# Optimization experiments

Hardware: AMD Instinct MI355X
Metric: run time of the kernel (lower is better)

Reference implementation:

```python
import jax, jax.numpy as jnp
import numpy as np

N_NODES = 50000
N_EDGES = 600000
D_IN, F1, F2, F3, D_OUT = 128, 128, 64, 64, 32
N_GRAPHS = 512


def setup_inputs() -> dict:
    key = jax.random.key(0)
    ks = jax.random.split(key, 16)
    x = jax.random.normal(ks[0], (N_NODES, D_IN), dtype=jnp.float32)
    edge_index = jax.random.randint(ks[1], (2, N_EDGES), 0, N_NODES, dtype=jnp.int64)
    batch = jnp.sort(jax.random.randint(ks[2], (N_NODES,), 0, N_GRAPHS, dtype=jnp.int64))

    def lin(k, fan_in, fan_out):
        bound = 1.0 / np.sqrt(fan_in)
        return jax.random.uniform(k, (fan_out, fan_in), jnp.float32, -bound, bound)

    return {
        "x": x, "edge_index": edge_index, "batch": batch,
        "w1_rel": lin(ks[3], D_IN, F1), "b1": jnp.zeros((F1,), jnp.float32), "w1_root": lin(ks[4], D_IN, F1),
        "w2_rel": lin(ks[5], F1, F2), "b2": jnp.zeros((F2,), jnp.float32), "w2_root": lin(ks[6], F1, F2),
        "w3_rel": lin(ks[7], F2, F3), "b3": jnp.zeros((F3,), jnp.float32), "w3_root": lin(ks[8], F2, F3),
        "fc1_w": lin(ks[9], F3, F3), "fc1_b": jnp.zeros((F3,), jnp.float32),
        "fc2_w": lin(ks[10], F3, D_OUT), "fc2_b": jnp.zeros((D_OUT,), jnp.float32),
    }


def graph_conv(x, src, dst, w_rel, b_rel, w_root):
    # GraphConv: out_i = W_rel @ (sum_{j->i} x_j) + b + W_root @ x_i
    aggr = jax.ops.segment_sum(x[src], dst, num_segments=x.shape[0])  # [N, d]
    return aggr @ w_rel.T + b_rel + x @ w_root.T


def reference(x, edge_index, batch,
              w1_rel, b1, w1_root, w2_rel, b2, w2_root, w3_rel, b3, w3_root,
              fc1_w, fc1_b, fc2_w, fc2_b):
    src, dst = edge_index[0], edge_index[1]
    h = jax.nn.relu(graph_conv(x, src, dst, w1_rel, b1, w1_root))
    h = jax.nn.relu(graph_conv(h, src, dst, w2_rel, b2, w2_root))
    h = graph_conv(h, src, dst, w3_rel, b3, w3_root)
    # global_add_pool over graphs in the batch
    g = jax.ops.segment_sum(h, batch, num_segments=N_GRAPHS)  # [G, F3]
    t = jax.nn.relu(g @ fc1_w.T + fc1_b)
    scores = t @ fc2_w.T + fc2_b
    return jax.nn.log_softmax(scores, axis=-1)
```

## Files before the change

### kernel.cpp

```cpp
#include <hip/hip_runtime.h>

#define N_NODES  50000
#define N_EDGES  600000
#define N_GRAPHS 512

#define SCAN_N   (N_NODES + 1)
#define SCAN_BPB 1024
#define SCAN_NB  ((SCAN_N + SCAN_BPB - 1) / SCAN_BPB)

#define F2BF_BLOCKS 6250
#define ZR_BLOCKS   196
#define WC_BLOCKS   224
#define ZG_BLOCKS   128

typedef __attribute__((ext_vector_type(8))) short bf16x8;
typedef __attribute__((ext_vector_type(4))) float f32x4;

static __device__ __forceinline__ unsigned f2bf(float f) {
    unsigned u = __float_as_uint(f);
    return (u + 0x7FFFu + ((u >> 16) & 1u)) >> 16;
}
static __device__ __forceinline__ float bflo(unsigned v) { return __uint_as_float(v << 16); }
static __device__ __forceinline__ float bfhi(unsigned v) { return __uint_as_float(v & 0xFFFF0000u); }

static __device__ __forceinline__ void addv8(float* acc, uint4 v) {
    acc[0] += bflo(v.x); acc[1] += bfhi(v.x);
    acc[2] += bflo(v.y); acc[3] += bfhi(v.y);
    acc[4] += bflo(v.z); acc[5] += bfhi(v.z);
    acc[6] += bflo(v.w); acc[7] += bfhi(v.w);
}
static __device__ __forceinline__ uint4 packv8(const float* f) {
    uint4 o;
    o.x = f2bf(f[0]) | (f2bf(f[1]) << 16);
    o.y = f2bf(f[2]) | (f2bf(f[3]) << 16);
    o.z = f2bf(f[4]) | (f2bf(f[5]) << 16);
    o.w = f2bf(f[6]) | (f2bf(f[7]) << 16);
    return o;
}


__global__ void init_kernel(const float* __restrict__ x, uint2* __restrict__ xb,
                            int* __restrict__ rowptr,
                            const float* __restrict__ w1r, const float* __restrict__ w1o,
                            const float* __restrict__ w2r, const float* __restrict__ w2o,
                            const float* __restrict__ w3r, const float* __restrict__ w3o,
                            unsigned short* __restrict__ wdst, float* __restrict__ G) {
    int b = blockIdx.x, t = threadIdx.x;
    if (b < F2BF_BLOCKS) {
        int i = b * 256 + t;
        float4 v = ((const float4*)x)[i];
        uint2 o;
        o.x = f2bf(v.x) | (f2bf(v.y) << 16);
        o.y = f2bf(v.z) | (f2bf(v.w) << 16);
        xb[i] = o;
    } else if (b < F2BF_BLOCKS + ZR_BLOCKS) {
        int i = (b - F2BF_BLOCKS) * 256 + t;
        if (i < SCAN_N) rowptr[i] = 0;
    } else if (b < F2BF_BLOCKS + ZR_BLOCKS + WC_BLOCKS) {
        int i = (b - F2BF_BLOCKS - ZR_BLOCKS) * 256 + t;
        const float* src; int off;
        if      (i < 16384) { src = w1r; off = 0; }
        else if (i < 32768) { src = w1o; off = 16384; }
        else if (i < 40960) { src = w2r; off = 32768; }
        else if (i < 49152) { src = w2o; off = 40960; }
        else if (i < 53248) { src = w3r; off = 49152; }
        else if (i < 57344) { src = w3o; off = 53248; }
        else return;
        wdst[i] = (unsigned short)f2bf(src[i - off]);
    } else {
        int i = (b - F2BF_BLOCKS - ZR_BLOCKS - WC_BLOCKS) * 256 + t;
        G[i] = 0.f;
    }
}


__global__ void hist_kernel(const int* __restrict__ edge, int* __restrict__ rowptr) {
    int e = blockIdx.x * blockDim.x + threadIdx.x;
    if (e < N_EDGES) atomicAdd(&rowptr[edge[N_EDGES + e] + 1], 1);
}

__global__ void scan_reduce_kernel(const int* __restrict__ data, int* __restrict__ bsum) {
    __shared__ int red[256];
    int b = blockIdx.x, t = threadIdx.x;
    int base = b * SCAN_BPB + t * 4;
    int s = 0;
#pragma unroll
    for (int j = 0; j < 4; ++j) {
        int idx = base + j;
        if (idx < SCAN_N) s += data[idx];
    }
    red[t] = s;
    __syncthreads();
    for (int off = 128; off > 0; off >>= 1) {
        if (t < off) red[t] += red[t + off];
        __syncthreads();
    }
    if (t == 0) bsum[b] = red[0];
}

__global__ void scan_apply_kernel(int* __restrict__ data, const int* __restrict__ bsum,
                                  int* __restrict__ cursor) {
    __shared__ int th[256];
    __shared__ int boff;
    int b = blockIdx.x, t = threadIdx.x;
    if (t == 0) {
        int run = 0;
        for (int i = 0; i < b; ++i) run += bsum[i];
        boff = run;
    }
    int base = b * SCAN_BPB + t * 4;
    int v[4];
    int s = 0;
#pragma unroll
    for (int j = 0; j < 4; ++j) {
        int idx = base + j;
        v[j] = (idx < SCAN_N) ? data[idx] : 0;
        s += v[j];
    }
    th[t] = s;
    __syncthreads();
    for (int off = 1; off < 256; off <<= 1) {
        int x = (t >= off) ? th[t - off] : 0;
        __syncthreads();
        th[t] += x;
        __syncthreads();
    }
    int run = boff + th[t] - s;
#pragma unroll
    for (int j = 0; j < 4; ++j) {
        int idx = base + j;
        run += v[j];
        if (idx < SCAN_N) {
            data[idx] = run;
            if (idx < N_NODES) cursor[idx] = run;
        }
    }
}

__global__ void scatter_kernel(const int* __restrict__ edge, int* __restrict__ cursor,
                               int* __restrict__ csr) {
    int e = blockIdx.x * blockDim.x + threadIdx.x;
    if (e < N_EDGES) {
        int d = edge[N_EDGES + e];
        int p = atomicAdd(&cursor[d], 1);
        csr[p] = edge[e];
    }
}


template <int LPN>
__global__ void aggregate_root(const unsigned short* __restrict__ Xb,
                               const int* __restrict__ rowptr,
                               const int* __restrict__ csr,
                               const unsigned short* __restrict__ ROOT,
                               unsigned short* __restrict__ OUT) {
    constexpr int NPB = 256 / LPN;
    int grp = threadIdx.x / LPN, lane = threadIdx.x % LPN;
    int i = blockIdx.x * NPB + grp;
    if (i >= N_NODES) return;
    const uint4* __restrict__ X4 = (const uint4*)Xb;
    int s = rowptr[i], e = rowptr[i + 1];
    float a[8] = {0.f}, b[8] = {0.f};
    int p = s;
    for (; p + 4 <= e; p += 4) {
        uint4 v0 = X4[(size_t)csr[p + 0] * LPN + lane];
        uint4 v1 = X4[(size_t)csr[p + 1] * LPN + lane];
        uint4 v2 = X4[(size_t)csr[p + 2] * LPN + lane];
        uint4 v3 = X4[(size_t)csr[p + 3] * LPN + lane];
        addv8(a, v0); addv8(b, v1); addv8(a, v2); addv8(b, v3);
    }
    if (p + 2 <= e) {
        uint4 v0 = X4[(size_t)csr[p] * LPN + lane];
        uint4 v1 = X4[(size_t)csr[p + 1] * LPN + lane];
        addv8(a, v0); addv8(b, v1);
        p += 2;
    }
    if (p < e) {
        uint4 v = X4[(size_t)csr[p] * LPN + lane];
        addv8(a, v);
    }
    float f[8];
#pragma unroll
    for (int k = 0; k < 8; ++k) f[k] = a[k] + b[k];
    uint4 r = ((const uint4*)ROOT)[(size_t)i * LPN + lane];
    f[0] += bflo(r.x); f[1] += bfhi(r.x);
    f[2] += bflo(r.y); f[3] += bfhi(r.y);
    f[4] += bflo(r.z); f[5] += bfhi(r.z);
    f[6] += bflo(r.w); f[7] += bfhi(r.w);
    ((uint4*)OUT)[(size_t)i * LPN + lane] = packv8(f);
}

__launch_bounds__(256, 2)
__global__ void fused_l1(const unsigned short* __restrict__ XB,
                         const int* __restrict__ rowptr, const int* __restrict__ csr,
                         const unsigned short* __restrict__ W1,
                         const unsigned short* __restrict__ W2,
                         const float* __restrict__ bias,
                         unsigned short* __restrict__ OUT) {
    __shared__ unsigned short aggr[64 * 128];
    const int tid = threadIdx.x;
    const int i0 = blockIdx.x * 64;

    {
        const uint4* __restrict__ X4 = (const uint4*)XB;
        int grp = tid >> 4, lane = tid & 15;
        for (int j = 0; j < 4; ++j) {
            int row = grp * 4 + j;
            int i = i0 + row;
            if (i >= N_NODES) break;
            int s = rowptr[i], e = rowptr[i + 1];
            float a[8] = {0.f}, b[8] = {0.f};
            int p = s;
            for (; p + 4 <= e; p += 4) {
                uint4 v0 = X4[(size_t)csr[p + 0] * 16 + lane];
                uint4 v1 = X4[(size_t)csr[p + 1] * 16 + lane];
                uint4 v2 = X4[(size_t)csr[p + 2] * 16 + lane];
                uint4 v3 = X4[(size_t)csr[p + 3] * 16 + lane];
                addv8(a, v0); addv8(b, v1); addv8(a, v2); addv8(b, v3);
            }
            if (p + 2 <= e) {
                uint4 v0 = X4[(size_t)csr[p] * 16 + lane];
                uint4 v1 = X4[(size_t)csr[p + 1] * 16 + lane];
                addv8(a, v0); addv8(b, v1);
                p += 2;
            }
            if (p < e) { uint4 v = X4[(size_t)csr[p] * 16 + lane]; addv8(a, v); }
            float f[8];
#pragma unroll
            for (int k = 0; k < 8; ++k) f[k] = a[k] + b[k];
            *(uint4*)&aggr[(row * 16 + (lane ^ (row & 7))) * 8] = packv8(f);
        }
    }
    const int l = tid & 63, wv = tid >> 6;
    const int lm = l & 15, lk = l >> 4;
    const int colbase = wv * 32;
    bf16x8 wf[2][8];
#pragma unroll
    for (int t = 0; t < 2; ++t) {
        int wrow = colbase + t * 16 + lm;
#pragma unroll
        for (int ks = 0; ks < 4; ++ks)
            wf[t][ks] = *(const bf16x8*)(W1 + (size_t)wrow * 128 + ks * 32 + lk * 8);
#pragma unroll
        for (int ks = 0; ks < 4; ++ks)
            wf[t][4 + ks] = *(const bf16x8*)(W2 + (size_t)wrow * 128 + ks * 32 + lk * 8);
    }
    __syncthreads();
    for (int r = 0; r < 4; ++r) {
        int rt = blockIdx.x * 4 + r;
        if (rt >= N_NODES / 16) break;
        f32x4 acc0 = (f32x4){0.f, 0.f, 0.f, 0.f};
        f32x4 acc1 = (f32x4){0.f, 0.f, 0.f, 0.f};
        int ldsrow = r * 16 + lm;
#pragma unroll
        for (int ks = 0; ks < 4; ++ks) {
            int c = ks * 4 + lk;
            bf16x8 a = *(const bf16x8*)&aggr[(ldsrow * 16 + (c ^ (ldsrow & 7))) * 8];
            acc0 = __builtin_amdgcn_mfma_f32_16x16x32_bf16(a, wf[0][ks], acc0, 0, 0, 0);
            acc1 = __builtin_amdgcn_mfma_f32_16x16x32_bf16(a, wf[1][ks], acc1, 0, 0, 0);
        }
        const unsigned short* a2row = XB + (size_t)(rt * 16 + lm) * 128 + lk * 8;
#pragma unroll
        for (int ks = 0; ks < 4; ++ks) {
            bf16x8 a = *(const bf16x8*)(a2row + ks * 32);
            acc0 = __builtin_amdgcn_mfma_f32_16x16x32_bf16(a, wf[0][4 + ks], acc0, 0, 0, 0);
            acc1 = __builtin_amdgcn_mfma_f32_16x16x32_bf16(a, wf[1][4 + ks], acc1, 0, 0, 0);
        }
#pragma unroll
        for (int t = 0; t < 2; ++t) {
            int n = colbase + t * 16 + lm;
            float bv = bias[n];
            const f32x4& acc = t ? acc1 : acc0;
#pragma unroll
            for (int jj = 0; jj < 4; ++jj) {
                int m = rt * 16 + lk * 4 + jj;
                float v = fmaxf(acc[jj] + bv, 0.f);
                OUT[(size_t)m * 128 + n] = (unsigned short)f2bf(v);
            }
        }
    }
}

template <int KS>
__launch_bounds__(256, 2)
__global__ void gemm_dual(const unsigned short* __restrict__ A,
                          const unsigned short* __restrict__ W,
                          const float* __restrict__ bias,
                          unsigned short* __restrict__ OUTY,
                          unsigned short* __restrict__ OUTR) {
    constexpr int K = KS * 32, NT = 2;
    const int l  = threadIdx.x & 63;
    const int wv = threadIdx.x >> 6;
    const int lm = l & 15, lk = l >> 4;
    const int colbase = wv * (NT * 16);

    bf16x8 wf[NT][KS];
#pragma unroll
    for (int t = 0; t < NT; ++t) {
        int wrow = colbase + t * 16 + lm;
#pragma unroll
        for (int ks = 0; ks < KS; ++ks)
            wf[t][ks] = *(const bf16x8*)(W + (size_t)wrow * K + ks * 32 + lk * 8);
    }

    int rt0 = blockIdx.x * 4;
    for (int r = 0; r < 4; ++r) {
        int rt = rt0 + r;
        if (rt >= N_NODES / 16) break;
        f32x4 acc[NT];
#pragma unroll
        for (int t = 0; t < NT; ++t) acc[t] = (f32x4){0.f, 0.f, 0.f, 0.f};

        const unsigned short* arow = A + (size_t)(rt * 16 + lm) * K + lk * 8;
#pragma unroll
        for (int ks = 0; ks < KS; ++ks) {
            bf16x8 a = *(const bf16x8*)(arow + ks * 32);
#pragma unroll
            for (int t = 0; t < NT; ++t)
                acc[t] = __builtin_amdgcn_mfma_f32_16x16x32_bf16(a, wf[t][ks], acc[t], 0, 0, 0);
        }
#pragma unroll
        for (int t = 0; t < NT; ++t) {
            int n = colbase + t * 16 + lm;
#pragma unroll
            for (int j = 0; j < 4; ++j) {
                int m = rt * 16 + lk * 4 + j;
                float v = acc[t][j];
                if (n < 64) {
                    OUTY[(size_t)m * 64 + n] = (unsigned short)f2bf(v);
                } else {
                    v += bias[n - 64];
                    OUTR[(size_t)m * 64 + (n - 64)] = (unsigned short)f2bf(v);
                }
            }
        }
    }
}

__launch_bounds__(256, 2)
__global__ void fused_l3(const unsigned short* __restrict__ Y2B,
                         const unsigned short* __restrict__ ROOT2,
                         const int* __restrict__ rowptr, const int* __restrict__ csr,
                         const unsigned short* __restrict__ W,
                         const float* __restrict__ bias,
                         unsigned short* __restrict__ OUTY,
                         unsigned short* __restrict__ OUTR) {
    __shared__ unsigned short h2[64 * 64];
    const int tid = threadIdx.x;
    const int i0 = blockIdx.x * 64;

    {
        const uint4* __restrict__ X4 = (const uint4*)Y2B;
        int grp = tid >> 3, lane = tid & 7;
        for (int j = 0; j < 2; ++j) {
            int row = grp * 2 + j;
            int i = i0 + row;
            if (i >= N_NODES) break;
            int s = rowptr[i], e = rowptr[i + 1];
            float a[8] = {0.f}, b[8] = {0.f};
            int p = s;
            for (; p + 4 <= e; p += 4) {
                uint4 v0 = X4[(size_t)csr[p + 0] * 8 + lane];
                uint4 v1 = X4[(size_t)csr[p + 1] * 8 + lane];
                uint4 v2 = X4[(size_t)csr[p + 2] * 8 + lane];
                uint4 v3 = X4[(size_t)csr[p + 3] * 8 + lane];
                addv8(a, v0); addv8(b, v1); addv8(a, v2); addv8(b, v3);
            }
            if (p + 2 <= e) {
                uint4 v0 = X4[(size_t)csr[p] * 8 + lane];
                uint4 v1 = X4[(size_t)csr[p + 1] * 8 + lane];
                addv8(a, v0); addv8(b, v1);
                p += 2;
            }
            if (p < e) { uint4 v = X4[(size_t)csr[p] * 8 + lane]; addv8(a, v); }
            float f[8];
#pragma unroll
            for (int k = 0; k < 8; ++k) f[k] = a[k] + b[k];
            uint4 rr = ((const uint4*)ROOT2)[(size_t)i * 8 + lane];
            f[0] += bflo(rr.x); f[1] += bfhi(rr.x);
            f[2] += bflo(rr.y); f[3] += bfhi(rr.y);
            f[4] += bflo(rr.z); f[5] += bfhi(rr.z);
            f[6] += bflo(rr.w); f[7] += bfhi(rr.w);
#pragma unroll
            for (int k = 0; k < 8; ++k) f[k] = fmaxf(f[k], 0.f);
            *(uint4*)&h2[(row * 8 + (lane ^ (row & 7))) * 8] = packv8(f);
        }
    }
    const int l = tid & 63, wv = tid >> 6;
    const int lm = l & 15, lk = l >> 4;
    const int colbase = wv * 32;
    bf16x8 wf[2][2];
#pragma unroll
    for (int t = 0; t < 2; ++t) {
        int wrow = colbase + t * 16 + lm;
#pragma unroll
        for (int ks = 0; ks < 2; ++ks)
            wf[t][ks] = *(const bf16x8*)(W + (size_t)wrow * 64 + ks * 32 + lk * 8);
    }
    __syncthreads();
    for (int r = 0; r < 4; ++r) {
        int rt = blockIdx.x * 4 + r;
        if (rt >= N_NODES / 16) break;
        f32x4 acc0 = (f32x4){0.f, 0.f, 0.f, 0.f};
        f32x4 acc1 = (f32x4){0.f, 0.f, 0.f, 0.f};
        int ldsrow = r * 16 + lm;
#pragma unroll
        for (int ks = 0; ks < 2; ++ks) {
            int c = ks * 4 + lk;
            bf16x8 a = *(const bf16x8*)&h2[(ldsrow * 8 + (c ^ (ldsrow & 7))) * 8];
            acc0 = __builtin_amdgcn_mfma_f32_16x16x32_bf16(a, wf[0][ks], acc0, 0, 0, 0);
            acc1 = __builtin_amdgcn_mfma_f32_16x16x32_bf16(a, wf[1][ks], acc1, 0, 0, 0);
        }
#pragma unroll
        for (int t = 0; t < 2; ++t) {
            int n = colbase + t * 16 + lm;
            const f32x4& acc = t ? acc1 : acc0;
#pragma unroll
            for (int jj = 0; jj < 4; ++jj) {
                int m = rt * 16 + lk * 4 + jj;
                float v = acc[jj];
                if (n < 64) {
                    OUTY[(size_t)m * 64 + n] = (unsigned short)f2bf(v);
                } else {
                    v += bias[n - 64];
                    OUTR[(size_t)m * 64 + (n - 64)] = (unsigned short)f2bf(v);
                }
            }
        }
    }
}


__global__ void pool_graph(const unsigned short* __restrict__ H,
                           const int* __restrict__ batch, float* __restrict__ G) {
    int g = blockIdx.x;
    int t = threadIdx.x;
    int lo = 0, hi = N_NODES;
    while (lo < hi) { int mid = (lo + hi) >> 1; if (batch[mid] < g) lo = mid + 1; else hi = mid; }
    int start = lo;
    hi = N_NODES;
    while (lo < hi) { int mid = (lo + hi) >> 1; if (batch[mid] < g + 1) lo = mid + 1; else hi = mid; }
    int end = lo;
    float acc = 0.f;
    for (int i = start; i < end; ++i)
        acc += __uint_as_float((unsigned)H[(size_t)i * 64 + t] << 16);
    G[(size_t)g * 64 + t] = acc;
}


__global__ void mlp_head(const float* __restrict__ G, const float* __restrict__ fc1w,
                         const float* __restrict__ fc1b, const float* __restrict__ fc2w,
                         const float* __restrict__ fc2b, float* __restrict__ out) {
    int g = blockIdx.x;
    int t = threadIdx.x;
    __shared__ float gr[64], tt[64], sc[32], red[2];
    gr[t] = G[(size_t)g * 64 + t];
    __syncthreads();
    float acc = fc1b[t];
#pragma unroll
    for (int k = 0; k < 64; ++k) acc += gr[k] * fc1w[t * 64 + k];
    tt[t] = fmaxf(acc, 0.f);
    __syncthreads();
    if (t < 32) {
        float s = fc2b[t];
#pragma unroll
        for (int k = 0; k < 64; ++k) s += tt[k] * fc2w[t * 64 + k];
        sc[t] = s;
    }
    __syncthreads();
    if (t == 0) {
        float mx = sc[0];
        for (int c = 1; c < 32; ++c) mx = fmaxf(mx, sc[c]);
        float sum = 0.f;
        for (int c = 0; c < 32; ++c) sum += expf(sc[c] - mx);
        red[0] = mx; red[1] = logf(sum);
    }
    __syncthreads();
    if (t < 32) out[(size_t)g * 32 + t] = sc[t] - red[0] - red[1];
}


extern "C" void kernel_launch(void* const* d_in, const int* in_sizes, int n_in,
                              void* d_out, int out_size, void* d_ws, size_t ws_size,
                              hipStream_t stream) {
    const float* x       = (const float*)d_in[0];
    const int*   edge    = (const int*)d_in[1];
    const int*   batch   = (const int*)d_in[2];
    const float* w1_rel  = (const float*)d_in[3];
    const float* b1      = (const float*)d_in[4];
    const float* w1_root = (const float*)d_in[5];
    const float* w2_rel  = (const float*)d_in[6];
    const float* b2      = (const float*)d_in[7];
    const float* w2_root = (const float*)d_in[8];
    const float* w3_rel  = (const float*)d_in[9];
    const float* b3      = (const float*)d_in[10];
    const float* w3_root = (const float*)d_in[11];
    const float* fc1w    = (const float*)d_in[12];
    const float* fc1b    = (const float*)d_in[13];
    const float* fc2w    = (const float*)d_in[14];
    const float* fc2b    = (const float*)d_in[15];
    float* out = (float*)d_out;

    char* p = (char*)d_ws;
    size_t used = 0;
    auto alloc = [&](size_t bytes) {
        char* r = p + used;
        used += (bytes + 255) & ~(size_t)255;
        return r;
    };
    int*            rowptr = (int*)alloc((N_NODES + 1) * sizeof(int));
    int*            cursor = (int*)alloc(N_NODES * sizeof(int));
    int*            csr    = (int*)alloc(N_EDGES * sizeof(int));
    int*            bsum   = (int*)alloc(SCAN_NB * sizeof(int));
    unsigned short* wbf    = (unsigned short*)alloc(57344 * sizeof(unsigned short));
    unsigned short* bufX   = (unsigned short*)alloc((size_t)N_NODES * 128 * 2);
    unsigned short* bufA   = (unsigned short*)alloc((size_t)N_NODES * 128 * 2);
    unsigned short* bufH   = (unsigned short*)alloc((size_t)N_NODES * 128 * 2);
    float*          G      = (float*)alloc((size_t)N_GRAPHS * 64 * sizeof(float));

    if (used > ws_size) return;

    unsigned short* w1r_bf = wbf;
    unsigned short* w1o_bf = wbf + 16384;
    unsigned short* w2cat  = wbf + 32768;
    unsigned short* w3cat  = wbf + 49152;

    unsigned short* XB    = bufX;
    unsigned short* H1b   = bufH;
    unsigned short* Y2B   = bufA;
    unsigned short* ROOT2 = bufA + (size_t)N_NODES * 64;
    unsigned short* Y3B   = bufX;
    unsigned short* ROOT3 = bufX + (size_t)N_NODES * 64;
    unsigned short* H3b   = bufH;

    init_kernel<<<F2BF_BLOCKS + ZR_BLOCKS + WC_BLOCKS + ZG_BLOCKS, 256, 0, stream>>>(
        x, (uint2*)XB, rowptr, w1_rel, w1_root, w2_rel, w2_root, w3_rel, w3_root, wbf, G);

    hist_kernel<<<(N_EDGES + 255) / 256, 256, 0, stream>>>(edge, rowptr);
    scan_reduce_kernel<<<SCAN_NB, 256, 0, stream>>>(rowptr, bsum);
    scan_apply_kernel<<<SCAN_NB, 256, 0, stream>>>(rowptr, bsum, cursor);
    scatter_kernel<<<(N_EDGES + 255) / 256, 256, 0, stream>>>(edge, cursor, csr);

    int gblk = (N_NODES + 63) / 64;

    fused_l1<<<gblk, 256, 0, stream>>>(XB, rowptr, csr, w1r_bf, w1o_bf, b1, H1b);

    gemm_dual<4><<<gblk, 256, 0, stream>>>(H1b, w2cat, b2, Y2B, ROOT2);

    fused_l3<<<gblk, 256, 0, stream>>>(Y2B, ROOT2, rowptr, csr, w3cat, b3, Y3B, ROOT3);

    aggregate_root<8><<<(N_NODES + 31) / 32, 256, 0, stream>>>(Y3B, rowptr, csr, ROOT3, H3b);

    pool_graph<<<N_GRAPHS, 64, 0, stream>>>(H3b, batch, G);
    mlp_head<<<N_GRAPHS, 64, 0, stream>>>(G, fc1w, fc1b, fc2w, fc2b, out);
}
```

Baseline: 303.2 us.

## Fuse final aggregation into graph pooling and store CSR indices as 16-bit

Replaces the separate layer-3 aggregate kernel and the per-graph pooling kernel with one kernel. It aggregates neighbours plus the root term and atomically adds each node's result into its graph's pooled vector. This removes the H3 intermediate write and read and one launch, at the cost of about 3.2M float atomics on G and nondeterministic summation order. The CSR source indices are also stored as unsigned short, which is valid because the node count is below 65536. That halves index traffic in every aggregation pass.

Measured after the change: 397.5 us. 31.1% more time.

```diff
diff --git a/kernel.cpp b/kernel.cpp
--- a/kernel.cpp
+++ b/kernel.cpp
@@ -138,61 +138,19 @@
 }
 
 __global__ void scatter_kernel(const int* __restrict__ edge, int* __restrict__ cursor,
-                               int* __restrict__ csr) {
+                               unsigned short* __restrict__ csr) {
     int e = blockIdx.x * blockDim.x + threadIdx.x;
     if (e < N_EDGES) {
         int d = edge[N_EDGES + e];
         int p = atomicAdd(&cursor[d], 1);
-        csr[p] = edge[e];
-    }
-}
-
-
-template <int LPN>
-__global__ void aggregate_root(const unsigned short* __restrict__ Xb,
-                               const int* __restrict__ rowptr,
-                               const int* __restrict__ csr,
-                               const unsigned short* __restrict__ ROOT,
-                               unsigned short* __restrict__ OUT) {
-    constexpr int NPB = 256 / LPN;
-    int grp = threadIdx.x / LPN, lane = threadIdx.x % LPN;
-    int i = blockIdx.x * NPB + grp;
-    if (i >= N_NODES) return;
-    const uint4* __restrict__ X4 = (const uint4*)Xb;
-    int s = rowptr[i], e = rowptr[i + 1];
-    float a[8] = {0.f}, b[8] = {0.f};
-    int p = s;
-    for (; p + 4 <= e; p += 4) {
-        uint4 v0 = X4[(size_t)csr[p + 0] * LPN + lane];
-        uint4 v1 = X4[(size_t)csr[p + 1] * LPN + lane];
-        uint4 v2 = X4[(size_t)csr[p + 2] * LPN + lane];
-        uint4 v3 = X4[(size_t)csr[p + 3] * LPN + lane];
-        addv8(a, v0); addv8(b, v1); addv8(a, v2); addv8(b, v3);
-    }
-    if (p + 2 <= e) {
-        uint4 v0 = X4[(size_t)csr[p] * LPN + lane];
-        uint4 v1 = X4[(size_t)csr[p + 1] * LPN + lane];
-        addv8(a, v0); addv8(b, v1);
-        p += 2;
-    }
-    if (p < e) {
-        uint4 v = X4[(size_t)csr[p] * LPN + lane];
-        addv8(a, v);
-    }
-    float f[8];
-#pragma unroll
-    for (int k = 0; k < 8; ++k) f[k] = a[k] + b[k];
-    uint4 r = ((const uint4*)ROOT)[(size_t)i * LPN + lane];
-    f[0] += bflo(r.x); f[1] += bfhi(r.x);
-    f[2] += bflo(r.y); f[3] += bfhi(r.y);
-    f[4] += bflo(r.z); f[5] += bfhi(r.z);
-    f[6] += bflo(r.w); f[7] += bfhi(r.w);
-    ((uint4*)OUT)[(size_t)i * LPN + lane] = packv8(f);
+        csr[p] = (unsigned short)edge[e];
+    }
 }
 
 __launch_bounds__(256, 2)
 __global__ void fused_l1(const unsigned short* __restrict__ XB,
-                         const int* __restrict__ rowptr, const int* __restrict__ csr,
+                         const int* __restrict__ rowptr,
+                         const unsigned short* __restrict__ csr,
                          const unsigned short* __restrict__ W1,
                          const unsigned short* __restrict__ W2,
                          const float* __restrict__ bias,
@@ -340,7 +298,8 @@
 __launch_bounds__(256, 2)
 __global__ void fused_l3(const unsigned short* __restrict__ Y2B,
                          const unsigned short* __restrict__ ROOT2,
-                         const int* __restrict__ rowptr, const int* __restrict__ csr,
+                         const int* __restrict__ rowptr,
+                         const unsigned short* __restrict__ csr,
                          const unsigned short* __restrict__ W,
                          const float* __restrict__ bias,
                          unsigned short* __restrict__ OUTY,
@@ -430,21 +389,45 @@
     }
 }
 
-
-__global__ void pool_graph(const unsigned short* __restrict__ H,
-                           const int* __restrict__ batch, float* __restrict__ G) {
-    int g = blockIdx.x;
-    int t = threadIdx.x;
-    int lo = 0, hi = N_NODES;
-    while (lo < hi) { int mid = (lo + hi) >> 1; if (batch[mid] < g) lo = mid + 1; else hi = mid; }
-    int start = lo;
-    hi = N_NODES;
-    while (lo < hi) { int mid = (lo + hi) >> 1; if (batch[mid] < g + 1) lo = mid + 1; else hi = mid; }
-    int end = lo;
-    float acc = 0.f;
-    for (int i = start; i < end; ++i)
-        acc += __uint_as_float((unsigned)H[(size_t)i * 64 + t] << 16);
-    G[(size_t)g * 64 + t] = acc;
+__global__ void aggregate_pool(const unsigned short* __restrict__ Y3B,
+                               const int* __restrict__ rowptr,
+                               const unsigned short* __restrict__ csr,
+                               const unsigned short* __restrict__ ROOT3,
+                               const int* __restrict__ batch,
+                               float* __restrict__ G) {
+    constexpr int LPN = 8;
+    int grp = threadIdx.x >> 3, lane = threadIdx.x & 7;
+    int i = blockIdx.x * 32 + grp;
+    if (i >= N_NODES) return;
+    const uint4* __restrict__ X4 = (const uint4*)Y3B;
+    int s = rowptr[i], e = rowptr[i + 1];
+    float a[8] = {0.f}, b[8] = {0.f};
+    int p = s;
+    for (; p + 4 <= e; p += 4) {
+        uint4 v0 = X4[(size_t)csr[p + 0] * LPN + lane];
+        uint4 v1 = X4[(size_t)csr[p + 1] * LPN + lane];
+        uint4 v2 = X4[(size_t)csr[p + 2] * LPN + lane];
+        uint4 v3 = X4[(size_t)csr[p + 3] * LPN + lane];
+        addv8(a, v0); addv8(b, v1); addv8(a, v2); addv8(b, v3);
+    }
+    if (p + 2 <= e) {
+        uint4 v0 = X4[(size_t)csr[p] * LPN + lane];
+        uint4 v1 = X4[(size_t)csr[p + 1] * LPN + lane];
+        addv8(a, v0); addv8(b, v1);
+        p += 2;
+    }
+    if (p < e) { uint4 v = X4[(size_t)csr[p] * LPN + lane]; addv8(a, v); }
+    float f[8];
+#pragma unroll
+    for (int k = 0; k < 8; ++k) f[k] = a[k] + b[k];
+    uint4 r = ((const uint4*)ROOT3)[(size_t)i * LPN + lane];
+    f[0] += bflo(r.x); f[1] += bfhi(r.x);
+    f[2] += bflo(r.y); f[3] += bfhi(r.y);
+    f[4] += bflo(r.z); f[5] += bfhi(r.z);
+    f[6] += bflo(r.w); f[7] += bfhi(r.w);
+    float* g = G + (size_t)batch[i] * 64 + lane * 8;
+#pragma unroll
+    for (int k = 0; k < 8; ++k) atomicAdd(&g[k], f[k]);
 }
 
 
@@ -510,7 +493,7 @@
     };
     int*            rowptr = (int*)alloc((N_NODES + 1) * sizeof(int));
     int*            cursor = (int*)alloc(N_NODES * sizeof(int));
-    int*            csr    = (int*)alloc(N_EDGES * sizeof(int));
+    unsigned short* csr    = (unsigned short*)alloc(N_EDGES * sizeof(unsigned short));
     int*            bsum   = (int*)alloc(SCAN_NB * sizeof(int));
     unsigned short* wbf    = (unsigned short*)alloc(57344 * sizeof(unsigned short));
     unsigned short* bufX   = (unsigned short*)alloc((size_t)N_NODES * 128 * 2);
@@ -531,7 +514,6 @@
     unsigned short* ROOT2 = bufA + (size_t)N_NODES * 64;
     unsigned short* Y3B   = bufX;
     unsigned short* ROOT3 = bufX + (size_t)N_NODES * 64;
-    unsigned short* H3b   = bufH;
 
     init_kernel<<<F2BF_BLOCKS + ZR_BLOCKS + WC_BLOCKS + ZG_BLOCKS, 256, 0, stream>>>(
         x, (uint2*)XB, rowptr, w1_rel, w1_root, w2_rel, w2_root, w3_rel, w3_root, wbf, G);
@@ -549,8 +531,7 @@
 
     fused_l3<<<gblk, 256, 0, stream>>>(Y2B, ROOT2, rowptr, csr, w3cat, b3, Y3B, ROOT3);
 
-    aggregate_root<8><<<(N_NODES + 31) / 32, 256, 0, stream>>>(Y3B, rowptr, csr, ROOT3, H3b);
-
-    pool_graph<<<N_GRAPHS, 64, 0, stream>>>(H3b, batch, G);
+    aggregate_pool<<<(N_NODES + 31) / 32, 256, 0, stream>>>(Y3B, rowptr, csr, ROOT3, batch, G);
+
     mlp_head<<<N_GRAPHS, 64, 0, stream>>>(G, fc1w, fc1b, fc2w, fc2b, out);
 }
```
